# Optimization experiments

Hardware: AMD Instinct MI355X
Metric: run time of the kernel (lower is better)

Reference implementation:

```python
import jax, jax.numpy as jnp
import numpy as np

# ---- static config (matches init_kwargs) ----
C = 1.0            # Lorentz curvature manifold.c
EPS_RMS = 1e-6     # LorentzRMSNorm eps
EPS_DEN = 1e-8     # centroid denominator clamp
B, S, DIM = 1, 2048, 2048
H = 16
NOPE, ROPE, VHD = 128, 65, 128   # qk_nope_head_dim, qk_rope_head_dim, v_head_dim
QK_HD = NOPE + ROPE              # 193 (full Lorentz q/k head dim incl. time)
KV_RANK = 512
ROPE_SP = ROPE - 1               # 64 = rotary space dim (even)
THETA = 10000.0


def _rotary(x, cos, sin):
    # x: (b, s, h, d) with d even; cos/sin: (s, d//2). Complex mult as real pairs.
    xr = x.reshape(*x.shape[:-1], -1, 2)
    x0, x1 = xr[..., 0], xr[..., 1]
    c = cos[None, :, None, :]
    s_ = sin[None, :, None, :]
    y = jnp.stack([x0 * c - x1 * s_, x0 * s_ + x1 * c], axis=-1)
    return y.reshape(*x.shape)


def _project(x_space):
    # lift space coords onto the Lorentz hyperboloid: prepend time = sqrt(|x|^2 + c)
    t = jnp.sqrt(jnp.sum(x_space * x_space, axis=-1, keepdims=True) + C)
    return jnp.concatenate([t, x_space], axis=-1)


def setup_inputs() -> dict:
    key = jax.random.key(0)
    ks = jax.random.split(key, 8)
    x = jax.random.normal(ks[0], (B, S, DIM), dtype=jnp.float32)
    # rotary tables over the 64-dim rope space (32 frequency pairs)
    freqs = 1.0 / (THETA ** (jnp.arange(0, ROPE_SP, 2, dtype=jnp.float32) / ROPE_SP))
    ang = jnp.arange(S, dtype=jnp.float32)[:, None] * freqs[None, :]   # (S, 32)
    freqs_cos, freqs_sin = jnp.cos(ang), jnp.sin(ang)
    mask = jnp.triu(jnp.ones((S, S), dtype=bool), k=1)  # True = masked (causal)
    w = 0.02
    wq_w = jax.random.normal(ks[1], (DIM, H * (QK_HD - 1)), dtype=jnp.float32) * w
    wkv_a_w = jax.random.normal(ks[2], (DIM, KV_RANK + ROPE - 1), dtype=jnp.float32) * w
    kv_norm_w = jnp.ones((KV_RANK,), dtype=jnp.float32)
    wkv_b_w = jax.random.normal(ks[3], (KV_RANK + 1, H * (NOPE + VHD - 1)), dtype=jnp.float32) * w
    wo_w = jax.random.normal(ks[4], (H * VHD, DIM - 1), dtype=jnp.float32) * w
    softmax_scale = jnp.array([np.sqrt(H * QK_HD)], dtype=jnp.float32)
    bias_p = jnp.zeros((), dtype=jnp.float32)
    return {"x": x, "start_pos": 0, "freqs_cos": freqs_cos, "freqs_sin": freqs_sin,
            "mask": mask, "wq_w": wq_w, "wkv_a_w": wkv_a_w, "kv_norm_w": kv_norm_w,
            "wkv_b_w": wkv_b_w, "wo_w": wo_w, "softmax_scale": softmax_scale,
            "bias_p": bias_p}


def reference(x, start_pos, freqs_cos, freqs_sin, mask, wq_w, wkv_a_w, kv_norm_w,
              wkv_b_w, wo_w, softmax_scale, bias_p):
    b, s, _ = x.shape
    # q projection (q_lora_rank == 0 path), space part only
    q = (x @ wq_w).reshape(b, s, H, QK_HD - 1)
    q_nope, q_pe = q[..., :NOPE], q[..., NOPE:]
    q_pe = _rotary(q_pe, freqs_cos, freqs_sin)
    q = jnp.concatenate([q_nope, q_pe], axis=-1)          # (b,s,H,QK_HD-1)
    # low-rank kv latent + rope key part
    kv_full = x @ wkv_a_w                                  # (b,s,KV_RANK+ROPE-1)
    kv, k_pe = kv_full[..., :KV_RANK], kv_full[..., KV_RANK:]
    k_pe = _rotary(k_pe[:, :, None, :], freqs_cos, freqs_sin)  # (b,s,1,64)
    # Lorentz RMSNorm (space_only): RMS-normalize space, scale, lift to hyperboloid
    rms = jnp.sqrt(jnp.mean(kv * kv, axis=-1, keepdims=True) + EPS_RMS)
    kv_pt = _project((kv / rms) * kv_norm_w)               # (b,s,KV_RANK+1)
    kvb = (kv_pt @ wkv_b_w).reshape(b, s, H, NOPE + VHD - 1)
    k_nope, v = kvb[..., :NOPE], kvb[..., NOPE:]
    k = jnp.concatenate([k_nope, jnp.broadcast_to(k_pe, (b, s, H, ROPE_SP))], axis=-1)
    # lift q/k to Lorentz points, Lorentz inner-product scores
    qs = _project(q).transpose(0, 2, 1, 3)                 # (b,H,s,QK_HD)
    ks_ = _project(k).transpose(0, 2, 1, 3)
    signs = jnp.concatenate([-jnp.ones((1,), x.dtype), jnp.ones((QK_HD - 1,), x.dtype)])
    scores = 2.0 * C + 2.0 * jnp.einsum('bhqd,bhkd->bhqk', qs * signs, ks_)
    scores = scores / softmax_scale + bias_p
    scores = jnp.where(mask[None, None], -1e18, scores)
    attn = jax.nn.softmax(scores.astype(jnp.float32), axis=-1).astype(x.dtype)
    # Lorentzian centroid of value points under attention weights
    vs = _project(v).transpose(0, 2, 1, 3)                 # (b,H,s,VHD)
    ave = jnp.einsum('bhqk,bhkd->bhqd', attn, vs)
    inner = -(ave[..., :1] ** 2) + jnp.sum(ave[..., 1:] ** 2, axis=-1, keepdims=True)
    cen = jnp.sqrt(C) * ave / jnp.sqrt(jnp.clip(jnp.abs(inner), EPS_DEN, None))
    out = cen.transpose(0, 2, 1, 3).reshape(b, s, H * VHD)
    return _project(out @ wo_w)                            # (b,s,DIM)
```

## Files before the change

### kernel.cpp

```cpp
#include <hip/hip_runtime.h>
#include <math.h>


typedef unsigned short u16;
typedef unsigned int u32;
typedef __attribute__((ext_vector_type(8))) short bf16x8;
typedef __attribute__((ext_vector_type(4))) float f32x4;

#define S_LEN 2048
#define NH 16
#define DPAD 224

__device__ __forceinline__ u16 f2bf(float f){
  u32 u = __builtin_bit_cast(u32, f);
  u32 r = u + 0x7fffu + ((u >> 16) & 1u);
  return (u16)(r >> 16);
}
__device__ __forceinline__ float bf2f(u16 h){
  u32 u = ((u32)h) << 16;
  return __builtin_bit_cast(float, u);
}

__global__ __launch_bounds__(256) void cast_bf16x8(
    const float* __restrict__ in, u16* __restrict__ out)
{
  size_t i = ((size_t)blockIdx.x*256 + threadIdx.x)*8;
  float4 a = *(const float4*)(in + i);
  float4 b = *(const float4*)(in + i + 4);
  uint4 v;
  v.x = (u32)f2bf(a.x) | ((u32)f2bf(a.y) << 16);
  v.y = (u32)f2bf(a.z) | ((u32)f2bf(a.w) << 16);
  v.z = (u32)f2bf(b.x) | ((u32)f2bf(b.y) << 16);
  v.w = (u32)f2bf(b.z) | ((u32)f2bf(b.w) << 16);
  *(uint4*)(out + i) = v;
}

__global__ void transpose_cast(const float* __restrict__ in, u16* __restrict__ out,
                               int R, int Cc, int outR, int outC)
{
  __shared__ float t[32][33];
  const int tx = threadIdx.x, ty = threadIdx.y;
  const int bx = blockIdx.x*32, by = blockIdx.y*32;
  #pragma unroll
  for (int i=0;i<4;++i){
    int r = bx + ty + i*8, c = by + tx;
    t[ty+i*8][tx] = (r<R && c<Cc) ? in[(size_t)r*Cc + c] : 0.f;
  }
  __syncthreads();
  #pragma unroll
  for (int i=0;i<4;++i){
    int orow = by + ty + i*8, ocol = bx + tx;
    if (orow<outR && ocol<outC) out[(size_t)orow*outC + ocol] = f2bf(t[tx][ty+i*8]);
  }
}

__global__ __launch_bounds__(256) void gemm_bf16(
    const u16* __restrict__ A, const u16* __restrict__ BT, u16* __restrict__ C,
    int M, int N, int K)
{
  __shared__ __align__(16) u16 As[128*32];
  __shared__ __align__(16) u16 Bs[128*32];
  const int tid = threadIdx.x;
  const int bm = blockIdx.y*128, bn = blockIdx.x*128;
  const int w = tid>>6, lane = tid&63, lg = lane>>4, li = lane&15;
  const int wr = w>>1, wc = w&1;
  const int srow = tid>>2, q = tid&3;
  const int swz = (q ^ (srow&3)) << 3;

  const u16* Ap  = A  + (size_t)(bm+srow)*K + q*8;
  const u16* Ap2 = Ap + (size_t)64*K;
  const u16* Bp  = BT + (size_t)(bn+srow)*K + q*8;
  const u16* Bp2 = Bp + (size_t)64*K;
  u16* aw  = &As[srow*32 + swz];
  u16* aw2 = &As[(srow+64)*32 + swz];
  u16* bw  = &Bs[srow*32 + swz];
  u16* bw2 = &Bs[(srow+64)*32 + swz];
  const int rsw = (lg ^ (li&3)) << 3;
  const u16* ar = &As[(wr*64+li)*32 + rsw];
  const u16* br = &Bs[(wc*64+li)*32 + rsw];

  f32x4 acc[4][4];
  #pragma unroll
  for (int m=0;m<4;++m)
    #pragma unroll
    for (int n=0;n<4;++n) acc[m][n] = (f32x4){0.f,0.f,0.f,0.f};

  const int nk = K >> 5;
  bf16x8 ra  = *(const bf16x8*)Ap;
  bf16x8 ra2 = *(const bf16x8*)Ap2;
  bf16x8 rb  = *(const bf16x8*)Bp;
  bf16x8 rb2 = *(const bf16x8*)Bp2;
  for (int kt=0; kt<nk; ++kt){
    __syncthreads();
    *(bf16x8*)aw = ra;  *(bf16x8*)aw2 = ra2;
    *(bf16x8*)bw = rb;  *(bf16x8*)bw2 = rb2;
    __syncthreads();
    if (kt+1 < nk){
      const int ko = (kt+1)*32;
      ra  = *(const bf16x8*)(Ap+ko);  ra2 = *(const bf16x8*)(Ap2+ko);
      rb  = *(const bf16x8*)(Bp+ko);  rb2 = *(const bf16x8*)(Bp2+ko);
    }
    bf16x8 af[4], bg[4];
    #pragma unroll
    for (int m=0;m<4;++m) af[m] = *(const bf16x8*)(ar + m*16*32);
    #pragma unroll
    for (int n=0;n<4;++n) bg[n] = *(const bf16x8*)(br + n*16*32);
    #pragma unroll
    for (int m=0;m<4;++m)
      #pragma unroll
      for (int n=0;n<4;++n)
        acc[m][n] = __builtin_amdgcn_mfma_f32_16x16x32_bf16(af[m], bg[n], acc[m][n], 0,0,0);
  }
  #pragma unroll
  for (int m=0;m<4;++m){
    const int row = bm + wr*64 + m*16 + lg*4;
    #pragma unroll
    for (int n=0;n<4;++n){
      const int col = bn + wc*64 + n*16 + li;
      #pragma unroll
      for (int r=0;r<4;++r)
        C[(size_t)(row+r)*N + col] = f2bf(acc[m][n][r]);
    }
  }
}

__global__ __launch_bounds__(256) void build_kvpt(
    const u16* __restrict__ kvfull,
    const float* __restrict__ gamma,
    const float* __restrict__ fc, const float* __restrict__ fs,
    u16* __restrict__ kvpt,
    float* __restrict__ kpe)
{
  const int s = blockIdx.x, tid = threadIdx.x;
  const int wv = tid>>6, lane = tid&63;
  const u16* src = kvfull + (size_t)s*640;
  __shared__ float red1[4], red2[4];
  float v0 = bf2f(src[tid]), v1 = bf2f(src[tid+256]);
  float sq = v0*v0 + v1*v1;
  #pragma unroll
  for (int off=32; off; off>>=1) sq += __shfl_down(sq, off);
  if (lane==0) red1[wv]=sq;
  __syncthreads();
  float tot = red1[0]+red1[1]+red1[2]+red1[3];
  float rinv = 1.0f/sqrtf(tot*(1.0f/512.0f)+1e-6f);
  float n0 = v0*rinv*gamma[tid], n1 = v1*rinv*gamma[tid+256];
  float s2 = n0*n0+n1*n1;
  #pragma unroll
  for (int off=32; off; off>>=1) s2 += __shfl_down(s2, off);
  if (lane==0) red2[wv]=s2;
  __syncthreads();
  u16* dst = kvpt + (size_t)s*544;
  dst[1+tid]   = f2bf(n0);
  dst[257+tid] = f2bf(n1);
  if (tid==0) dst[0] = f2bf(sqrtf(red2[0]+red2[1]+red2[2]+red2[3]+1.0f));
  if (tid<31) dst[513+tid] = 0;
  if (tid<32){
    float x0 = bf2f(src[512+2*tid]), x1 = bf2f(src[513+2*tid]);
    float c = fc[(size_t)s*32+tid], sn = fs[(size_t)s*32+tid];
    kpe[(size_t)s*64 + 2*tid]   = x0*c - x1*sn;
    kpe[(size_t)s*64 + 2*tid+1] = x0*sn + x1*c;
  }
}

__global__ __launch_bounds__(64) void build_qproj(
    const u16* __restrict__ qraw,
    const float* __restrict__ fc, const float* __restrict__ fs,
    u16* __restrict__ qp)
{
  const int s = blockIdx.x, h = blockIdx.y, lane = threadIdx.x;
  const u16* src = qraw + (size_t)s*3072 + h*192;
  u16* dst = qp + ((size_t)h*S_LEN + s)*DPAD;
  u16 e0 = src[lane], e1 = src[lane+64];
  float f0 = bf2f(e0), f1 = bf2f(e1);
  dst[1+lane] = e0; dst[65+lane] = e1;
  float sq = f0*f0 + f1*f1;
  if (lane < 32){
    float x0 = bf2f(src[128+2*lane]), x1 = bf2f(src[129+2*lane]);
    float c = fc[(size_t)s*32+lane], sn = fs[(size_t)s*32+lane];
    float y0 = x0*c - x1*sn, y1 = x0*sn + x1*c;
    dst[129+2*lane] = f2bf(y0); dst[130+2*lane] = f2bf(y1);
    sq += y0*y0 + y1*y1;
  }
  if (lane < 31) dst[193+lane] = 0;
  #pragma unroll
  for (int off=32; off; off>>=1) sq += __shfl_down(sq, off);
  if (lane==0) dst[0] = f2bf(-sqrtf(sq+1.0f));
}

__global__ __launch_bounds__(64) void build_kvproj(
    const u16* __restrict__ kvb,
    const float* __restrict__ kpe,
    u16* __restrict__ kp,
    u16* __restrict__ vt)
{
  const int s = blockIdx.x, h = blockIdx.y, lane = threadIdx.x;
  const u16* src = kvb + (size_t)s*4096 + h*255;
  u16* kdst = kp + ((size_t)h*S_LEN + s)*DPAD;
  u16 a0 = src[lane], a1 = src[lane+64];
  float fa0 = bf2f(a0), fa1 = bf2f(a1);
  float pe = kpe[(size_t)s*64 + lane];
  kdst[1+lane] = a0; kdst[65+lane] = a1; kdst[129+lane] = f2bf(pe);
  if (lane<31) kdst[193+lane] = 0;
  float sq = fa0*fa0 + fa1*fa1 + pe*pe;
  #pragma unroll
  for (int off=32; off; off>>=1) sq += __shfl_down(sq, off);
  if (lane==0) kdst[0] = f2bf(sqrtf(sq+1.0f));
  u16 b0 = src[128+lane];
  u16 b1 = (lane<63) ? src[192+lane] : (u16)0;
  float fb0 = bf2f(b0), fb1 = bf2f(b1);
  u16* vbase = vt + (size_t)h*128*S_LEN;
  vbase[(size_t)(1+lane)*S_LEN + s] = b0;
  if (lane<63) vbase[(size_t)(65+lane)*S_LEN + s] = b1;
  float sv = fb0*fb0 + fb1*fb1;
  #pragma unroll
  for (int off=32; off; off>>=1) sv += __shfl_down(sv, off);
  if (lane==0) vbase[s] = f2bf(sqrtf(sv+1.0f));
}

__global__ __launch_bounds__(256) void attn_part(
    const u16* __restrict__ qp,
    const u16* __restrict__ kp,
    const u16* __restrict__ vt,
    const float* __restrict__ ss,
    float* __restrict__ Opart,
    float* __restrict__ ml)
{
  const int h  = blockIdx.x & 15;
  const int ub = blockIdx.x >> 4;
  const int w = threadIdx.x>>6, lane = threadIdx.x&63;
  const int u = ub*4 + w;
  int c = 0, rem = u;
  while (rem >= 128 - 16*c){ rem -= 128 - 16*c; ++c; }
  const int s16 = c*16 + rem;
  const int lg = lane>>4, li = lane&15;
  const int r0 = s16*16;
  const float cl2 = (2.0f/ss[0]) * 1.44269504088896f;
  __shared__ __align__(16) u16 P[4][16][72];

  const u16* qb = qp + ((size_t)h*S_LEN + r0 + li)*DPAD + lg*8;
  bf16x8 qf[7];
  #pragma unroll
  for (int d=0; d<7; ++d) qf[d] = *(const bf16x8*)(qb + d*32);

  f32x4 of[8];
  #pragma unroll
  for (int d=0; d<8; ++d) of[d] = (f32x4){0.f,0.f,0.f,0.f};
  float mreg[4] = {-3e38f,-3e38f,-3e38f,-3e38f};
  float lreg[4] = {0.f,0.f,0.f,0.f};

  const int t0 = c*4;
  const int tE = min(c*4+3, (r0+15)>>6);
  for (int t=t0; t<=tE; ++t){
    const int k0 = t*64;
    const u16* kb = kp + ((size_t)h*S_LEN + k0 + li)*DPAD + lg*8;
    f32x4 s[4];
    #pragma unroll
    for (int j=0;j<4;++j) s[j] = (f32x4){0.f,0.f,0.f,0.f};
    #pragma unroll
    for (int d=0; d<7; ++d){
      #pragma unroll
      for (int j=0;j<4;++j){
        bf16x8 kf = *(const bf16x8*)(kb + j*16*DPAD + d*32);
        s[j] = __builtin_amdgcn_mfma_f32_16x16x32_bf16(qf[d], kf, s[j], 0,0,0);
      }
    }
    const u16* vb = vt + ((size_t)h*128 + li)*S_LEN + k0 + lg*8;
    bf16x8 vlo[8];
    #pragma unroll
    for (int d=0;d<8;++d) vlo[d] = *(const bf16x8*)(vb + (size_t)d*16*S_LEN);

    float alpha[4];
    #pragma unroll
    for (int r=0;r<4;++r){
      const int row = r0 + lg*4 + r;
      float a0 = (k0 + li      <= row) ? s[0][r] : -3e38f;
      float a1 = (k0 + 16 + li <= row) ? s[1][r] : -3e38f;
      float a2 = (k0 + 32 + li <= row) ? s[2][r] : -3e38f;
      float a3 = (k0 + 48 + li <= row) ? s[3][r] : -3e38f;
      float mx = fmaxf(fmaxf(a0,a1), fmaxf(a2,a3));
      mx = fmaxf(mx, __shfl_xor(mx,1));
      mx = fmaxf(mx, __shfl_xor(mx,2));
      mx = fmaxf(mx, __shfl_xor(mx,4));
      mx = fmaxf(mx, __shfl_xor(mx,8));
      float mn = fmaxf(mreg[r], mx);
      alpha[r] = exp2f((mreg[r]-mn)*cl2);
      mreg[r] = mn;
      float e0 = exp2f((a0-mn)*cl2);
      float e1 = exp2f((a1-mn)*cl2);
      float e2 = exp2f((a2-mn)*cl2);
      float e3 = exp2f((a3-mn)*cl2);
      float ls = (e0+e1)+(e2+e3);
      ls += __shfl_xor(ls,1);
      ls += __shfl_xor(ls,2);
      ls += __shfl_xor(ls,4);
      ls += __shfl_xor(ls,8);
      lreg[r] = lreg[r]*alpha[r] + ls;
      P[w][lg*4+r][li]    = f2bf(e0);
      P[w][lg*4+r][li+16] = f2bf(e1);
      P[w][lg*4+r][li+32] = f2bf(e2);
      P[w][lg*4+r][li+48] = f2bf(e3);
    }
    #pragma unroll
    for (int d=0;d<8;++d){
      of[d][0]*=alpha[0]; of[d][1]*=alpha[1];
      of[d][2]*=alpha[2]; of[d][3]*=alpha[3];
    }
    bf16x8 pa0 = *(const bf16x8*)(&P[w][li][lg*8]);
    bf16x8 pa1 = *(const bf16x8*)(&P[w][li][32+lg*8]);
    #pragma unroll
    for (int d=0;d<8;++d){
      bf16x8 vhi = *(const bf16x8*)(vb + (size_t)d*16*S_LEN + 32);
      of[d] = __builtin_amdgcn_mfma_f32_16x16x32_bf16(pa0, vlo[d], of[d], 0,0,0);
      of[d] = __builtin_amdgcn_mfma_f32_16x16x32_bf16(pa1, vhi,    of[d], 0,0,0);
    }
  }
  const int slot = h*576 + c*128 - (c*(c-1))*8 + (s16 - 16*c);
  float* ob = Opart + (size_t)slot*2048;
  #pragma unroll
  for (int r=0;r<4;++r){
    const int rw = lg*4 + r;
    #pragma unroll
    for (int d=0;d<8;++d) ob[(size_t)rw*128 + d*16 + li] = of[d][r];
    if (li == 0){
      ml[((size_t)slot*16 + rw)*2]   = mreg[r];
      ml[((size_t)slot*16 + rw)*2+1] = lreg[r];
    }
  }
}

__global__ __launch_bounds__(256) void attn_combine(
    const float* __restrict__ Opart, const float* __restrict__ ml,
    const float* __restrict__ ss, u16* __restrict__ out)
{
  const int h = blockIdx.x & 15;
  const int s16 = blockIdx.x >> 4;
  const int nc = (s16 >> 4) + 1;
  const int tid = threadIdx.x;
  const int row = tid >> 4;
  const int ci  = tid & 15;
  const float cl2 = (2.0f/ss[0]) * 1.44269504088896f;

  int slot[8];
  #pragma unroll
  for (int c=0;c<8;++c) slot[c] = h*576 + c*128 - (c*(c-1))*8 + (s16 - 16*c);

  float m[8], l[8];
  float mstar = -3e38f;
  #pragma unroll
  for (int c=0;c<8;++c){
    if (c < nc){
      float2 v = *(const float2*)(ml + ((size_t)slot[c]*16 + row)*2);
      m[c] = v.x; l[c] = v.y;
    } else { m[c] = -3e38f; l[c] = 0.f; }
    mstar = fmaxf(mstar, m[c]);
  }
  float lstar = 0.f; float wgt[8];
  #pragma unroll
  for (int c=0;c<8;++c){ wgt[c] = exp2f((m[c]-mstar)*cl2); lstar += l[c]*wgt[c]; }
  float linv = 1.0f/lstar;

  float av[8];
  float o[8] = {0.f,0.f,0.f,0.f,0.f,0.f,0.f,0.f};
  #pragma unroll
  for (int c=0;c<8;++c){
    if (c < nc){
      const float* pb = Opart + (size_t)slot[c]*2048 + row*128 + ci*8;
      float4 p0 = *(const float4*)(pb);
      float4 p1 = *(const float4*)(pb+4);
      o[0] += p0.x*wgt[c]; o[1] += p0.y*wgt[c]; o[2] += p0.z*wgt[c]; o[3] += p0.w*wgt[c];
      o[4] += p1.x*wgt[c]; o[5] += p1.y*wgt[c]; o[6] += p1.z*wgt[c]; o[7] += p1.w*wgt[c];
    }
  }
  float part = 0.f;
  #pragma unroll
  for (int j=0;j<8;++j){ av[j] = o[j]*linv; part += av[j]*av[j]; }
  if (ci==0) part -= 2.f*av[0]*av[0];
  part += __shfl_xor(part,1);
  part += __shfl_xor(part,2);
  part += __shfl_xor(part,4);
  part += __shfl_xor(part,8);
  float sc = 1.0f/sqrtf(fmaxf(fabsf(part),1e-8f));
  u16* ob = out + (size_t)(s16*16+row)*2048 + h*128 + ci*8;
  #pragma unroll
  for (int j=0;j<8;++j) ob[j] = f2bf(av[j]*sc);
}

__global__ __launch_bounds__(256) void final_project(
    const u16* __restrict__ y,
    float* __restrict__ out)
{
  const int s = blockIdx.x, tid = threadIdx.x;
  const int wv = tid>>6, lane = tid&63;
  const u16* src = y + (size_t)s*2048;
  float* dst = out + (size_t)s*2048;
  float sq = 0.f;
  for (int j=tid; j<2047; j+=256){
    float v = bf2f(src[j]);
    dst[1+j] = v;
    sq += v*v;
  }
  __shared__ float red[4];
  #pragma unroll
  for (int off=32; off; off>>=1) sq += __shfl_down(sq, off);
  if (lane==0) red[wv]=sq;
  __syncthreads();
  if (tid==0) dst[0] = sqrtf(red[0]+red[1]+red[2]+red[3]+1.0f);
}

extern "C" void kernel_launch(void* const* d_in, const int* in_sizes, int n_in,
                              void* d_out, int out_size, void* d_ws, size_t ws_size,
                              hipStream_t stream) {
  const float* x    = (const float*)d_in[0];
  const float* fc   = (const float*)d_in[2];
  const float* fs   = (const float*)d_in[3];
  const float* wq   = (const float*)d_in[5];
  const float* wkva = (const float*)d_in[6];
  const float* gam  = (const float*)d_in[7];
  const float* wkvb = (const float*)d_in[8];
  const float* wo   = (const float*)d_in[9];
  const float* ssp  = (const float*)d_in[10];
  float* out = (float*)d_out;
  char* base = (char*)d_ws;

  u16*   xb     = (u16*)(base + 0);
  u16*   wqT    = (u16*)(base + 8388608);
  u16*   wkvaT  = (u16*)(base + 20971520);
  u16*   wkvbT  = (u16*)(base + 23592960);
  u16*   kvfull = (u16*)(base + 28049408);
  u16*   kvpt   = (u16*)(base + 30670848);
  float* kpe    = (float*)(base + 32899072);
  u16*   kvb    = (u16*)(base + 33423360);
  u16*   qraw   = (u16*)(base + 69206016);
  u16*   qproj  = (u16*)(base + 81788928);
  u16*   kproj  = (u16*)(base + 96468992);
  u16*   vprojT = (u16*)(base + 111149056);
  float* Opart  = (float*)(base + 0);
  float* mlbuf  = (float*)(base + 75497472);
  u16*   attn_o = (u16*)(base + 76677120);
  u16*   woT    = (u16*)(base + 0);
  u16*   yb     = (u16*)(base + 8388608);

  dim3 tb(32,8);
  cast_bf16x8<<<2048, 256, 0, stream>>>(x, xb);
  transpose_cast<<<dim3(64,96),  tb, 0, stream>>>(wq,   wqT,   2048, 3072, 3072, 2048);
  transpose_cast<<<dim3(64,20),  tb, 0, stream>>>(wkva, wkvaT, 2048,  576,  640, 2048);
  gemm_bf16<<<dim3(24,16), 256, 0, stream>>>(xb, wqT,   qraw,   2048, 3072, 2048);
  gemm_bf16<<<dim3(5,16),  256, 0, stream>>>(xb, wkvaT, kvfull, 2048,  640, 2048);
  build_kvpt<<<2048, 256, 0, stream>>>(kvfull, gam, fc, fs, kvpt, kpe);
  transpose_cast<<<dim3(17,128), tb, 0, stream>>>(wkvb, wkvbT,  513, 4080, 4096,  544);
  gemm_bf16<<<dim3(32,16), 256, 0, stream>>>(kvpt, wkvbT, kvb,  2048, 4096,  544);
  build_qproj<<<dim3(2048,16), 64, 0, stream>>>(qraw, fc, fs, qproj);
  build_kvproj<<<dim3(2048,16), 64, 0, stream>>>(kvb, kpe, kproj, vprojT);
  attn_part<<<2304, 256, 0, stream>>>(qproj, kproj, vprojT, ssp, Opart, mlbuf);
  attn_combine<<<2048, 256, 0, stream>>>(Opart, mlbuf, ssp, attn_o);
  transpose_cast<<<dim3(64,64), tb, 0, stream>>>(wo, woT, 2048, 2047, 2048, 2048);
  gemm_bf16<<<dim3(16,16), 256, 0, stream>>>(attn_o, woT, yb, 2048, 2048, 2048);
  final_project<<<2048, 256, 0, stream>>>(yb, out);
}
```

Measured before the change: 484.1 us.

## Share K tiles across waves via swizzled LDS with register prefetch

Each block now covers one 64-row query strip, with its four waves working on adjacent 16-row sub-tiles, so the waves read the same key tiles. Each 64-key K tile is staged once into XOR-swizzled shared memory, and the next tile is prefetched into registers while the current one is used. This cuts redundant global K loads (previously each wave loaded K on its own). V loads move next to the PV MFMAs, setprio hints wrap the MFMA sections, and the slot indexing for partial outputs is remapped to match. The cost is added barriers, extra LDS and register pressure, and coarser causal load balance per block.

```diff
diff --git a/kernel.cpp b/kernel.cpp
--- a/kernel.cpp
+++ b/kernel.cpp
@@ -226,16 +226,26 @@
     float* __restrict__ ml)
 {
   const int h  = blockIdx.x & 15;
-  const int ub = blockIdx.x >> 4;
-  const int w = threadIdx.x>>6, lane = threadIdx.x&63;
-  const int u = ub*4 + w;
-  int c = 0, rem = u;
-  while (rem >= 128 - 16*c){ rem -= 128 - 16*c; ++c; }
-  const int s16 = c*16 + rem;
+  int ub = blockIdx.x >> 4;
+  int c = 0;
+  while (ub >= 32 - 4*c){ ub -= 32 - 4*c; ++c; }
+  const int strip = 4*c + ub;
+  const int tid = threadIdx.x;
+  const int w = tid>>6, lane = tid&63;
   const int lg = lane>>4, li = lane&15;
-  const int r0 = s16*16;
+  const int r0 = strip*64 + w*16;
   const float cl2 = (2.0f/ss[0]) * 1.44269504088896f;
+  __shared__ __align__(16) u16 Ks[64*256];
   __shared__ __align__(16) u16 P[4][16][72];
+
+  u16* dstp[7]; int rowv[7], ocv[7];
+  #pragma unroll
+  for (int i=0;i<7;++i){
+    int p = tid + i*256;
+    int r = p/28, oc = p - r*28;
+    rowv[i] = r; ocv[i] = oc;
+    dstp[i] = Ks + ((r*512 + ((oc*16) ^ ((r&7)<<4))) >> 1);
+  }
 
   const u16* qb = qp + ((size_t)h*S_LEN + r0 + li)*DPAD + lg*8;
   bf16x8 qf[7];
@@ -249,25 +259,43 @@
   float lreg[4] = {0.f,0.f,0.f,0.f};
 
   const int t0 = c*4;
-  const int tE = min(c*4+3, (r0+15)>>6);
+  const int tE = min(c*4+3, strip);
+  const u16* khead = kp + (size_t)h*S_LEN*DPAD;
+
+  bf16x8 kst[7];
+  {
+    const u16* kb0 = khead + (size_t)(t0*64)*DPAD;
+    #pragma unroll
+    for (int i=0;i<7;++i) kst[i] = *(const bf16x8*)(kb0 + (size_t)rowv[i]*DPAD + ocv[i]*8);
+  }
+
   for (int t=t0; t<=tE; ++t){
     const int k0 = t*64;
-    const u16* kb = kp + ((size_t)h*S_LEN + k0 + li)*DPAD + lg*8;
+    __syncthreads();
+    #pragma unroll
+    for (int i=0;i<7;++i) *(bf16x8*)dstp[i] = kst[i];
+    if (t < tE){
+      const u16* kbn = khead + (size_t)((t+1)*64)*DPAD;
+      #pragma unroll
+      for (int i=0;i<7;++i) kst[i] = *(const bf16x8*)(kbn + (size_t)rowv[i]*DPAD + ocv[i]*8);
+    }
+    asm volatile("s_waitcnt lgkmcnt(0)" ::: "memory");
+    __builtin_amdgcn_s_barrier();
+
     f32x4 s[4];
     #pragma unroll
     for (int j=0;j<4;++j) s[j] = (f32x4){0.f,0.f,0.f,0.f};
+    const int xs = (li&7)<<4;
+    __builtin_amdgcn_s_setprio(1);
     #pragma unroll
     for (int d=0; d<7; ++d){
       #pragma unroll
       for (int j=0;j<4;++j){
-        bf16x8 kf = *(const bf16x8*)(kb + j*16*DPAD + d*32);
+        const bf16x8 kf = *(const bf16x8*)(Ks + (((li + j*16)*512 + ((lg*16 + d*64) ^ xs)) >> 1));
         s[j] = __builtin_amdgcn_mfma_f32_16x16x32_bf16(qf[d], kf, s[j], 0,0,0);
       }
     }
-    const u16* vb = vt + ((size_t)h*128 + li)*S_LEN + k0 + lg*8;
-    bf16x8 vlo[8];
-    #pragma unroll
-    for (int d=0;d<8;++d) vlo[d] = *(const bf16x8*)(vb + (size_t)d*16*S_LEN);
+    __builtin_amdgcn_s_setprio(0);
 
     float alpha[4];
     #pragma unroll
@@ -307,14 +335,19 @@
     }
     bf16x8 pa0 = *(const bf16x8*)(&P[w][li][lg*8]);
     bf16x8 pa1 = *(const bf16x8*)(&P[w][li][32+lg*8]);
+    const u16* vb = vt + ((size_t)h*128 + li)*S_LEN + k0 + lg*8;
+    __builtin_amdgcn_s_setprio(1);
     #pragma unroll
     for (int d=0;d<8;++d){
-      bf16x8 vhi = *(const bf16x8*)(vb + (size_t)d*16*S_LEN + 32);
-      of[d] = __builtin_amdgcn_mfma_f32_16x16x32_bf16(pa0, vlo[d], of[d], 0,0,0);
-      of[d] = __builtin_amdgcn_mfma_f32_16x16x32_bf16(pa1, vhi,    of[d], 0,0,0);
-    }
-  }
-  const int slot = h*576 + c*128 - (c*(c-1))*8 + (s16 - 16*c);
+      bf16x8 vf0 = *(const bf16x8*)(vb + (size_t)d*16*S_LEN);
+      bf16x8 vf1 = *(const bf16x8*)(vb + (size_t)d*16*S_LEN + 32);
+      of[d] = __builtin_amdgcn_mfma_f32_16x16x32_bf16(pa0, vf0, of[d], 0,0,0);
+      of[d] = __builtin_amdgcn_mfma_f32_16x16x32_bf16(pa1, vf1, of[d], 0,0,0);
+    }
+    __builtin_amdgcn_s_setprio(0);
+  }
+
+  const int slot = (h*144 + 32*c - 2*c*(c-1) + (strip - 4*c))*4 + w;
   float* ob = Opart + (size_t)slot*2048;
   #pragma unroll
   for (int r=0;r<4;++r){
@@ -334,6 +367,7 @@
 {
   const int h = blockIdx.x & 15;
   const int s16 = blockIdx.x >> 4;
+  const int strip = s16 >> 2, wv = s16 & 3;
   const int nc = (s16 >> 4) + 1;
   const int tid = threadIdx.x;
   const int row = tid >> 4;
@@ -342,7 +376,8 @@
 
   int slot[8];
   #pragma unroll
-  for (int c=0;c<8;++c) slot[c] = h*576 + c*128 - (c*(c-1))*8 + (s16 - 16*c);
+  for (int c=0;c<8;++c)
+    slot[c] = (h*144 + 32*c - 2*c*(c-1) + (strip - 4*c))*4 + wv;
 
   float m[8], l[8];
   float mstar = -3e38f;
```

Measured after the change: 453.3 us. -6.4%, faster.
